# Kernel tuning notes

Measured on AMD Instinct MI355X. Metric: run time of the kernel, lower is better.

The kernel has to match this reference:

```python
import jax, jax.numpy as jnp
import numpy as np
from jax import lax

NMS_RADIUS = 4
THRESHOLD = 0.005
BORDER = 4
MAX_KP = 1024


def _max_pool(x, r):
    # torch max_pool2d pads with -inf; reduce_window 'SAME' pads with init value.
    w = 2 * r + 1
    return lax.reduce_window(x, -jnp.inf, lax.max, (1, w, w), (1, 1, 1), 'SAME')


def simple_nms(scores, radius):
    zeros = jnp.zeros_like(scores)
    max_mask = scores == _max_pool(scores, radius)
    for _ in range(2):
        supp_mask = _max_pool(max_mask.astype(scores.dtype), radius) > 0
        supp_scores = jnp.where(supp_mask, zeros, scores)
        new_max_mask = supp_scores == _max_pool(supp_scores, radius)
        max_mask = max_mask | (new_max_mask & ~supp_mask)
    return jnp.where(max_mask, scores, zeros)


def sample_descriptors(kp, desc, s):
    """Bilinear grid_sample (align_corners=True, zero padding) + L2 normalize.
    kp: [B,N,2] (x,y) full-resolution pixel coords; desc: [B,C,h,w]."""
    b, c, h, w = desc.shape
    k = kp - s / 2 + 0.5
    gx = k[..., 0] / (w * s - 1) * 2.0 - 1.0
    gy = k[..., 1] / (h * s - 1) * 2.0 - 1.0
    x = (gx + 1.0) * 0.5 * (w - 1)  # align_corners=True mapping
    y = (gy + 1.0) * 0.5 * (h - 1)
    x0 = jnp.floor(x); y0 = jnp.floor(y)
    wx1 = x - x0; wy1 = y - y0
    x0i = x0.astype(jnp.int32); y0i = y0.astype(jnp.int32)

    def tap(d_b, xi, yi):  # d_b [C,h,w]; xi,yi [N] -> [C,N], zero outside
        v = ((xi >= 0) & (xi < w) & (yi >= 0) & (yi < h)).astype(d_b.dtype)
        g = d_b[:, jnp.clip(yi, 0, h - 1), jnp.clip(xi, 0, w - 1)]
        return g * v

    def one(d_b, x0i, y0i, wx1, wy1):
        wx0 = 1.0 - wx1; wy0 = 1.0 - wy1
        return (tap(d_b, x0i, y0i) * (wx0 * wy0)
                + tap(d_b, x0i + 1, y0i) * (wx1 * wy0)
                + tap(d_b, x0i, y0i + 1) * (wx0 * wy1)
                + tap(d_b, x0i + 1, y0i + 1) * (wx1 * wy1))

    out = jax.vmap(one)(desc, x0i, y0i, wx1, wy1)  # [B,C,N]
    n = jnp.maximum(jnp.linalg.norm(out, axis=1, keepdims=True), 1e-12)
    return out / n


def conv1x1(w, b, x):  # Conv1d kernel_size=1: [O,I] @ [B,I,N]
    return jnp.einsum('oi,bin->bon', w, x) + b[None, :, None]


def setup_inputs() -> dict:
    key = jax.random.key(0)
    ks = jax.random.split(key, 13)
    B, H, W = 4, 480, 640
    inp = {
        'scores': jax.random.uniform(ks[0], (B, H, W), jnp.float32),
        'd1': jax.random.normal(ks[1], (B, 64, H // 2, W // 2), jnp.float32),
        'd2': jax.random.normal(ks[2], (B, 128, H // 4, W // 4), jnp.float32),
        'cDa': jax.random.normal(ks[3], (B, 256, H // 8, W // 8), jnp.float32),
        'd4': jax.random.normal(ks[4], (B, 256, H // 16, W // 16), jnp.float32),
        'lin0_w': jax.random.normal(ks[5], (256, 256), jnp.float32) / np.sqrt(256),
        'lin0_b': jax.random.normal(ks[6], (256,), jnp.float32) * 0.01,
        'lin1_w': jax.random.normal(ks[7], (128, 128), jnp.float32) / np.sqrt(128),
        'lin1_b': jax.random.normal(ks[8], (128,), jnp.float32) * 0.01,
        'lin2_w': jax.random.normal(ks[9], (64, 64), jnp.float32) / np.sqrt(64),
        'lin2_b': jax.random.normal(ks[10], (64,), jnp.float32) * 0.01,
        'merge_w': jax.random.normal(ks[11], (256, 704), jnp.float32) / np.sqrt(704),
        'merge_b': jax.random.normal(ks[12], (256,), jnp.float32) * 0.01,
    }
    return inp


def reference(scores, d1, d2, cDa, d4, lin0_w, lin0_b, lin1_w, lin1_b,
              lin2_w, lin2_b, merge_w, merge_b):
    B, H, W = scores.shape
    s = simple_nms(scores, NMS_RADIUS)
    ys, xs = jnp.meshgrid(jnp.arange(H), jnp.arange(W), indexing='ij')
    valid = (ys >= BORDER) & (ys < H - BORDER) & (xs >= BORDER) & (xs < W - BORDER)
    masked = jnp.where(valid[None] & (s > THRESHOLD), s, -1.0)
    top_scores, idx = lax.top_k(masked.reshape(B, -1), MAX_KP)
    kx = (idx % W).astype(jnp.float32)
    ky = (idx // W).astype(jnp.float32)
    kp = jnp.stack([kx, ky], axis=-1)  # [B,K,2] (x,y), i.e. torch.flip(k,[1])
    de1 = sample_descriptors(kp, d1, 2)    # [B,64,K]
    de2 = sample_descriptors(kp, d2, 4)    # [B,128,K]
    de3 = sample_descriptors(kp, cDa, 8)   # [B,256,K]
    de4 = sample_descriptors(kp, d4, 16)   # [B,256,K]
    de4 = conv1x1(lin0_w, lin0_b, de4)
    de2 = conv1x1(lin1_w, lin1_b, de2)
    de1 = conv1x1(lin2_w, lin2_b, de1)
    descriptors = conv1x1(merge_w, merge_b,
                          jnp.concatenate([de1, de2, de3, de4], axis=1))
    return kp, top_scores, descriptors
```

## Files before the change

kernel.cpp:

```cpp
#include <hip/hip_runtime.h>
#include <hip/hip_bf16.h>

#define B 4
#define H 480
#define W 640
#define HW (H*W)
#define BHW (B*H*W)
#define NKP 1024
#define THRESH 0.005f
#define CAP 16384
#define NCOL (B*NKP)
#define KTOT 704

typedef __attribute__((ext_vector_type(8))) short s8v;
typedef __attribute__((ext_vector_type(4))) float f4v;
typedef struct { float x, y; } __attribute__((aligned(4))) f2u;

__device__ __forceinline__ short f2bf(float f) {
    __hip_bfloat16 h = __float2bfloat16(f);
    return *(short*)&h;
}

__device__ __forceinline__ float max3f(float a, float b, float c) {
    return fmaxf(fmaxf(a, b), c);
}
#define MAX9(A, base, str) \
    max3f(max3f((A)[(base)], (A)[(base)+(str)], (A)[(base)+2*(str)]), \
          max3f((A)[(base)+3*(str)], (A)[(base)+4*(str)], (A)[(base)+5*(str)]), \
          max3f((A)[(base)+6*(str)], (A)[(base)+7*(str)], (A)[(base)+8*(str)]))

__global__ __launch_bounds__(256) void fuse_w(const float* __restrict__ merge_w,
                                              const float* __restrict__ lin0_w,
                                              const float* __restrict__ lin1_w,
                                              const float* __restrict__ lin2_w,
                                              short* __restrict__ Mw) {
    __shared__ float red[4][64];
    int lane = threadIdx.x & 63;
    int wv = threadIdx.x >> 6;
    int jb = blockIdx.x;
    int o = blockIdx.y;
    int j = jb * 64 + lane;
    const float* mwr = merge_w + (size_t)o * KTOT;

    if (jb >= 3 && jb <= 6) {
        if (wv == 0) Mw[(size_t)o * KTOT + j] = f2bf(mwr[j]);
        return;
    }
    float acc = 0.0f;
    if (jb == 0) {
        int k0 = wv * 16;
        #pragma unroll
        for (int k = 0; k < 16; ++k)
            acc += mwr[k0 + k] * lin2_w[(k0 + k) * 64 + lane];
    } else if (jb <= 2) {
        int jj = (jb - 1) * 64 + lane;
        int k0 = wv * 32;
        #pragma unroll
        for (int k = 0; k < 32; ++k)
            acc += mwr[64 + k0 + k] * lin1_w[(k0 + k) * 128 + jj];
    } else {
        int jj = (jb - 7) * 64 + lane;
        int k0 = wv * 64;
        #pragma unroll
        for (int k = 0; k < 64; ++k)
            acc += mwr[448 + k0 + k] * lin0_w[(k0 + k) * 256 + jj];
    }
    red[wv][lane] = acc;
    __syncthreads();
    if (wv == 0) {
        float t = red[0][lane] + red[1][lane] + red[2][lane] + red[3][lane];
        Mw[(size_t)o * KTOT + j] = f2bf(t);
    }
}

__global__ __launch_bounds__(256) void fuse_bias(const float* __restrict__ merge_w,
                                                 const float* __restrict__ merge_b,
                                                 const float* __restrict__ lin0_b,
                                                 const float* __restrict__ lin1_b,
                                                 const float* __restrict__ lin2_b,
                                                 float* __restrict__ biasf,
                                                 int* __restrict__ cnt) {
    int lane = threadIdx.x & 63;
    int wv = threadIdx.x >> 6;
    int o = blockIdx.x * 4 + wv;
    if (blockIdx.x == 0 && threadIdx.x < 4) cnt[threadIdx.x * 64] = 0;
    const float* mwr = merge_w + (size_t)o * KTOT;
    float acc = 0.0f;
    #pragma unroll
    for (int i = 0; i < 11; ++i) {
        int k = i * 64 + lane;
        float c;
        if (k < 64) c = lin2_b[k];
        else if (k < 192) c = lin1_b[k - 64];
        else if (k < 448) c = 0.0f;
        else c = lin0_b[k - 448];
        acc += mwr[k] * c;
    }
    #pragma unroll
    for (int off = 32; off > 0; off >>= 1) acc += __shfl_xor(acc, off, 64);
    if (lane == 0) biasf[o] = merge_b[o] + acc;
}

__global__ __launch_bounds__(256) void transpose_d4(const float* __restrict__ d4,
                                                    float* __restrict__ d4T) {
    __shared__ float T[64][65];
    int b = blockIdx.z;
    int p0 = blockIdx.x * 64;
    int c0 = blockIdx.y * 64;
    for (int t = threadIdx.x; t < 4096; t += 256) {
        int ch = t >> 6, px = t & 63;
        int gp = p0 + px;
        if (gp < 1200)
            T[ch][px] = d4[((size_t)(b * 256 + c0 + ch)) * 1200 + gp];
    }
    __syncthreads();
    for (int t = threadIdx.x; t < 4096; t += 256) {
        int px = t >> 6, ch = t & 63;
        int gp = p0 + px;
        if (gp < 1200)
            d4T[((size_t)(b * 1200 + gp)) * 256 + c0 + ch] = T[ch][px];
    }
}

__global__ __launch_bounds__(256) void transpose_cDa(const float* __restrict__ cDa,
                                                     float* __restrict__ cDaT) {
    __shared__ float T[64][65];
    int b = blockIdx.z;
    int p0 = blockIdx.x * 64;
    int c0 = blockIdx.y * 64;
    for (int t = threadIdx.x; t < 4096; t += 256) {
        int ch = t >> 6, px = t & 63;
        T[ch][px] = cDa[((size_t)(b * 256 + c0 + ch)) * 4800 + p0 + px];
    }
    __syncthreads();
    for (int t = threadIdx.x; t < 4096; t += 256) {
        int px = t >> 6, ch = t & 63;
        cDaT[((size_t)(b * 4800 + p0 + px)) * 256 + c0 + ch] = T[ch][px];
    }
}

__global__ __launch_bounds__(512) void nms_fused(const float* __restrict__ scores,
                                                 unsigned long long* __restrict__ cand,
                                                 int* __restrict__ cnt) {
    __shared__ float S72[72 * 72];
    __shared__ float T72[72 * 64];
    __shared__ float Mm[64 * 64];
    __shared__ float Zm[56 * 56];
    __shared__ int lcnt, gbase;
    int bz = blockIdx.z;
    int x0 = blockIdx.x * 32, y0 = blockIdx.y * 32;
    const float* sp = scores + bz * HW;
    if (threadIdx.x == 0) lcnt = 0;
    for (int t = threadIdx.x; t < 5184; t += 512) {
        int i = t / 72, j = t - i * 72;
        int gy = y0 - 20 + i, gx = x0 - 20 + j;
        S72[t] = (gy >= 0 && gy < H && gx >= 0 && gx < W) ? sp[gy * W + gx] : -1.0f;
    }
    __syncthreads();
    for (int t = threadIdx.x; t < 4608; t += 512) {
        int i = t >> 6, c = t & 63;
        T72[i * 64 + c] = MAX9(S72, i * 72 + c, 1);
    }
    __syncthreads();
    for (int t = threadIdx.x; t < 4096; t += 512) {
        int r = t >> 6, c = t & 63;
        float m = MAX9(T72, r * 64 + c, 64);
        float s = S72[(r + 4) * 72 + c + 4];
        int gy = y0 - 16 + r, gx = x0 - 16 + c;
        Mm[t] = (gy >= 0 && gy < H && gx >= 0 && gx < W && s == m) ? 1.0f : 0.0f;
    }
    __syncthreads();
    float* Tm = T72;
    for (int t = threadIdx.x; t < 3584; t += 512) {
        int i = t / 56, c = t - i * 56;
        Tm[i * 56 + c] = MAX9(Mm, i * 64 + c, 1);
    }
    __syncthreads();
    for (int t = threadIdx.x; t < 3136; t += 512) {
        int i = t / 56, j = t - i * 56;
        float m = MAX9(Tm, i * 56 + j, 56);
        Zm[t] = (m > 0.0f) ? -1.0f : S72[(i + 8) * 72 + (j + 8)];
    }
    __syncthreads();
    for (int t = threadIdx.x; t < 2688; t += 512) {
        int i = t / 48, c = t - i * 48;
        Tm[i * 56 + c] = MAX9(Zm, i * 56 + c, 1);
    }
    __syncthreads();
    for (int t = threadIdx.x; t < 2304; t += 512) {
        int r = t / 48, c = t - r * 48;
        float m = MAX9(Tm, r * 56 + c, 56);
        float Zc = Zm[(r + 4) * 56 + c + 4];
        int mi = (r + 8) * 64 + c + 8;
        bool nm = (Zc == m) && (Zc >= 0.0f);
        Mm[mi] = (Mm[mi] != 0.0f || nm) ? 1.0f : 0.0f;
    }
    __syncthreads();
    for (int t = threadIdx.x; t < 1920; t += 512) {
        int r = t / 40, c = t - r * 40;
        Tm[r * 56 + c] = MAX9(Mm, (r + 8) * 64 + c + 8, 1);
    }
    __syncthreads();
    for (int t = threadIdx.x; t < 1600; t += 512) {
        int r = t / 40, c = t - r * 40;
        float m = MAX9(Tm, r * 56 + c, 56);
        int zi = (r + 8) * 56 + c + 8;
        Zm[zi] = (m > 0.0f) ? -1.0f : S72[(r + 16) * 72 + (c + 16)];
    }
    __syncthreads();
    for (int t = threadIdx.x; t < 1280; t += 512) {
        int r = t / 32, c = t & 31;
        Tm[r * 56 + c] = MAX9(Zm, (r + 8) * 56 + c + 8, 1);
    }
    __syncthreads();
    unsigned long long keys[2];
    int nl = 0;
    #pragma unroll
    for (int q = 0; q < 2; ++q) {
        int t = threadIdx.x + q * 512;
        int r3 = t >> 5, c = t & 31;
        float m = MAX9(Tm, r3 * 56 + c, 56);
        float Zc = Zm[(r3 + 12) * 56 + c + 12];
        bool fin = (Mm[(r3 + 16) * 64 + c + 16] != 0.0f) || ((Zc == m) && (Zc >= 0.0f));
        int gy = y0 + r3, gx = x0 + c;
        float sc = S72[(r3 + 20) * 72 + (c + 20)];
        if (fin && gy >= 4 && gy < H - 4 && gx >= 4 && gx < W - 4 && sc > THRESH) {
            unsigned r = (unsigned)(gy * W + gx);
            unsigned bits = __float_as_uint(sc) | 0x80000000u;
            keys[nl++] = ((unsigned long long)bits << 32) |
                         (unsigned long long)(0xFFFFFFFFu - r);
        }
    }
    int lpos = 0;
    if (nl) lpos = atomicAdd(&lcnt, nl);
    __syncthreads();
    if (threadIdx.x == 0) gbase = (lcnt > 0) ? atomicAdd(&cnt[bz * 64], lcnt) : 0;
    __syncthreads();
    for (int j = 0; j < nl; ++j) {
        int p = gbase + lpos + j;
        if (p < CAP) cand[(size_t)bz * CAP + p] = keys[j];
    }
}

__global__ __launch_bounds__(1024) void topk(const unsigned long long* __restrict__ cand,
                                             const int* __restrict__ cnt,
                                             float* __restrict__ out, int* __restrict__ fidx,
                                             int* __restrict__ perm) {
    __shared__ int hist[2048];
    __shared__ int wtot[16], wcarry[16];
    __shared__ unsigned long long buf[4096];
    __shared__ int scnt, spiv1, spiv2, sabove;
    int b = blockIdx.x, tid = threadIdx.x;
    int lane = tid & 63, wv = tid >> 6;
    int m = cnt[b * 64]; if (m > CAP) m = CAP;
    const unsigned long long* cb = cand + (size_t)b * CAP;
    int target = (m < 1024) ? m : 1024;

    hist[tid] = 0; hist[tid + 1024] = 0;
    if (tid == 0) { scnt = 0; spiv1 = 2048; spiv2 = 0; sabove = 0; }
    __syncthreads();
    for (int i = tid; i < m; i += 1024)
        atomicAdd(&hist[(int)(cb[i] >> 53) & 0x7FF], 1);
    __syncthreads();
    {
        int base = wv * 128;
        int a = hist[base + lane];
        int c = hist[base + 64 + lane];
        int as = a, cs = c;
        #pragma unroll
        for (int off = 1; off < 64; off <<= 1) {
            int t1 = __shfl_down(as, off, 64);
            if (lane + off < 64) as += t1;
            int t2 = __shfl_down(cs, off, 64);
            if (lane + off < 64) cs += t2;
        }
        int ctot = __shfl(cs, 0, 64);
        as += ctot;
        if (lane == 0) wtot[wv] = as;
        __syncthreads();
        if (wv == 0 && lane < 16) {
            int v = wtot[lane];
            #pragma unroll
            for (int off = 1; off < 16; off <<= 1) {
                int t1 = __shfl_down(v, off, 64);
                if (lane + off < 16) v += t1;
            }
            wcarry[lane] = v - wtot[lane];
        }
        __syncthreads();
        int carry = wcarry[wv];
        hist[base + lane] = as + carry;
        hist[base + 64 + lane] = cs + carry;
    }
    __syncthreads();
    if (target > 0) {
        for (int t = tid; t < 2048; t += 1024) {
            int c = hist[t];
            int cn = (t < 2047) ? hist[t + 1] : 0;
            if (c >= target && cn < target) { spiv1 = t; sabove = cn; }
        }
    }
    __syncthreads();
    int piv1 = spiv1;
    int target2 = target - sabove;
    hist[tid] = 0; hist[tid + 1024] = 0;
    __syncthreads();
    for (int i = tid; i < m; i += 1024) {
        unsigned long long k = cb[i];
        if (((int)(k >> 53) & 0x7FF) == piv1)
            atomicAdd(&hist[(int)(k >> 42) & 0x7FF], 1);
    }
    __syncthreads();
    {
        int base = wv * 128;
        int a = hist[base + lane];
        int c = hist[base + 64 + lane];
        int as = a, cs = c;
        #pragma unroll
        for (int off = 1; off < 64; off <<= 1) {
            int t1 = __shfl_down(as, off, 64);
            if (lane + off < 64) as += t1;
            int t2 = __shfl_down(cs, off, 64);
            if (lane + off < 64) cs += t2;
        }
        int ctot = __shfl(cs, 0, 64);
        as += ctot;
        if (lane == 0) wtot[wv] = as;
        __syncthreads();
        if (wv == 0 && lane < 16) {
            int v = wtot[lane];
            #pragma unroll
            for (int off = 1; off < 16; off <<= 1) {
                int t1 = __shfl_down(v, off, 64);
                if (lane + off < 16) v += t1;
            }
            wcarry[lane] = v - wtot[lane];
        }
        __syncthreads();
        int carry = wcarry[wv];
        hist[base + lane] = as + carry;
        hist[base + 64 + lane] = cs + carry;
    }
    __syncthreads();
    if (target > 0) {
        for (int t = tid; t < 2048; t += 1024) {
            int c = hist[t];
            int cn = (t < 2047) ? hist[t + 1] : 0;
            if (c >= target2 && cn < target2) spiv2 = t;
        }
    }
    __syncthreads();
    int piv2 = spiv2;
    for (int i = tid; i < m; i += 1024) {
        unsigned long long k = cb[i];
        int b1 = (int)(k >> 53) & 0x7FF;
        bool sel = (target > 0) &&
                   (b1 > piv1 || (b1 == piv1 && (((int)(k >> 42) & 0x7FF) >= piv2)));
        if (sel) {
            int p = atomicAdd(&scnt, 1);
            if (p < 4096) buf[p] = k;
        }
    }
    __syncthreads();
    int sc_ = scnt; if (sc_ > 4096) sc_ = 4096;
    int ns = 1024; while (ns < sc_) ns <<= 1;
    for (int t = tid; t < ns; t += 1024) if (t >= sc_) buf[t] = 0ULL;
    __syncthreads();
    int nseg = ns >> 6;
    for (int seg = wv; seg < nseg; seg += 16) {
        int e = (seg << 6) + lane;
        unsigned long long v = buf[e];
        #pragma unroll
        for (int k = 2; k <= 64; k <<= 1) {
            #pragma unroll
            for (int j = k >> 1; j >= 1; j >>= 1) {
                unsigned long long p = __shfl_xor(v, j, 64);
                bool upper = (lane & j) != 0;
                bool dird = ((e & k) == 0);
                bool keepmax = (dird != upper);
                v = keepmax ? (v > p ? v : p) : (v < p ? v : p);
            }
        }
        buf[e] = v;
    }
    for (int k = 128; k <= ns; k <<= 1) {
        for (int j = k >> 1; j >= 64; j >>= 1) {
            __syncthreads();
            for (int t = tid; t < ns; t += 1024) {
                int ixj = t ^ j;
                if (ixj > t) {
                    unsigned long long a = buf[t], bb = buf[ixj];
                    if (((t & k) == 0) ? (a < bb) : (a > bb)) { buf[t] = bb; buf[ixj] = a; }
                }
            }
        }
        __syncthreads();
        for (int seg = wv; seg < nseg; seg += 16) {
            int e = (seg << 6) + lane;
            unsigned long long v = buf[e];
            #pragma unroll
            for (int j = 32; j >= 1; j >>= 1) {
                unsigned long long p = __shfl_xor(v, j, 64);
                bool upper = (lane & j) != 0;
                bool dird = ((e & k) == 0);
                bool keepmax = (dird != upper);
                v = keepmax ? (v > p ? v : p) : (v < p ? v : p);
            }
            buf[e] = v;
        }
    }
    __syncthreads();
    unsigned long long key = buf[tid];
    float kx, ky, sc;
    unsigned idx;
    if (key != 0ULL) {
        unsigned ord = (unsigned)(key >> 32);
        sc = __uint_as_float(ord ^ 0x80000000u);
        idx = 0xFFFFFFFFu - (unsigned)(key & 0xFFFFFFFFu);
        kx = (float)(idx % W);
        ky = (float)(idx / W);
    } else {
        sc = -1.0f; idx = 0; kx = 0.0f; ky = 0.0f;
    }
    int bn = b * NKP + tid;
    out[bn * 2 + 0] = kx;
    out[bn * 2 + 1] = ky;
    out[B * NKP * 2 + bn] = sc;
    fidx[bn] = (int)idx;
    __syncthreads();
    if (tid < 512) { hist[tid] = 0; hist[tid + 1024] = 0; }
    __syncthreads();
    int bucket = (int)(idx >> 10);
    atomicAdd(&hist[bucket], 1);
    __syncthreads();
    int iv = 0;
    if (wv < 8) {
        iv = hist[wv * 64 + lane];
        #pragma unroll
        for (int off = 1; off < 64; off <<= 1) {
            int t1 = __shfl_up(iv, off, 64);
            if (lane >= off) iv += t1;
        }
        if (lane == 63) wtot[wv] = iv;
    }
    __syncthreads();
    if (wv == 0 && lane < 8) {
        int v = wtot[lane], iv2 = v;
        #pragma unroll
        for (int off = 1; off < 8; off <<= 1) {
            int t1 = __shfl_up(iv2, off, 64);
            if (lane >= off) iv2 += t1;
        }
        wcarry[lane] = iv2 - v;
    }
    __syncthreads();
    if (wv < 8) hist[512 + wv * 64 + lane] = iv + wcarry[wv];
    __syncthreads();
    int intra = atomicAdd(&hist[1024 + bucket], 1);
    int pos = hist[512 + bucket] - hist[bucket] + intra;
    perm[b * NKP + pos] = tid;
}

__global__ __launch_bounds__(256) void sample_all(const float* __restrict__ d1,
                                                  const float* __restrict__ d2,
                                                  const float* __restrict__ cDa,
                                                  const float* __restrict__ d4T,
                                                  const float* __restrict__ cDaT,
                                                  const int* __restrict__ fidx,
                                                  const int* __restrict__ perm,
                                                  short* __restrict__ X) {
    int lane = threadIdx.x & 63;
    int wv = threadIdx.x >> 6;
    int seg = blockIdx.y;
    int bid = blockIdx.x;
    int swz = ((bid & 7) << 7) | (bid >> 3);
    int b = swz >> 8;
    int g0 = ((swz & 255) << 2) + wv;

    const float* map; int h, w, s, C, base, nset;
    if (seg == 0)      { map = d1;  h = 240; w = 320; s = 2;  C = 64;  base = 0;   nset = 1; }
    else if (seg == 1) { map = d2;  h = 120; w = 160; s = 4;  C = 128; base = 64;  nset = 2; }
    else if (seg == 2) { map = cDa; h = 60;  w = 80;  s = 8;  C = 256; base = 192; nset = 4; }
    else               { map = d4T; h = 30;  w = 40;  s = 16; C = 256; base = 448; nset = 4; }

    int col = (b << 10) | perm[(b << 10) + g0];
    int idx = fidx[col];
    float kx = (float)(idx % W);
    float ky = (float)(idx / W);
    float kxs = kx - (float)s * 0.5f + 0.5f;
    float kys = ky - (float)s * 0.5f + 0.5f;
    float gx = kxs / (float)(w * s - 1) * 2.0f - 1.0f;
    float gy = kys / (float)(h * s - 1) * 2.0f - 1.0f;
    float x = (gx + 1.0f) * 0.5f * (float)(w - 1);
    float y = (gy + 1.0f) * 0.5f * (float)(h - 1);
    float x0f = floorf(x), y0f = floorf(y);
    int x0 = (int)x0f, y0 = (int)y0f;
    float wx1 = x - x0f, wy1 = y - y0f;
    float wx0 = 1.0f - wx1, wy0 = 1.0f - wy1;
    bool vx0 = (x0 >= 0) && (x0 < w);
    bool vx1 = (x0 + 1 >= 0) && (x0 + 1 < w);
    bool vy0 = (y0 >= 0) && (y0 < h);
    bool vy1 = (y0 + 1 >= 0) && (y0 + 1 < h);
    int xc0 = min(max(x0, 0), w - 1), xc1 = min(max(x0 + 1, 0), w - 1);
    int yc0 = min(max(y0, 0), h - 1), yc1 = min(max(y0 + 1, 0), h - 1);
    float w00 = (vx0 && vy0) ? wx0 * wy0 : 0.0f;
    float w01 = (vx1 && vy0) ? wx1 * wy0 : 0.0f;
    float w10 = (vx0 && vy1) ? wx0 * wy1 : 0.0f;
    float w11 = (vx1 && vy1) ? wx1 * wy1 : 0.0f;

    bool nhwc = (seg == 3) || (seg == 2 && cDaT != nullptr);
    float vals[4];
    float r = 0.0f;
    if (nhwc) {
        const float* pt;
        int wq;
        if (seg == 3) { pt = d4T + ((size_t)b * 1200) * 256 + lane; wq = 40; }
        else          { pt = cDaT + ((size_t)b * 4800) * 256 + lane; wq = 80; }
        size_t o00 = ((size_t)(yc0 * wq + xc0)) << 8;
        size_t o01 = ((size_t)(yc0 * wq + xc1)) << 8;
        size_t o10 = ((size_t)(yc1 * wq + xc0)) << 8;
        size_t o11 = ((size_t)(yc1 * wq + xc1)) << 8;
        float q00[4], q01[4], q10[4], q11[4];
        #pragma unroll
        for (int j = 0; j < 4; ++j) {
            q00[j] = pt[o00 + j * 64]; q01[j] = pt[o01 + j * 64];
            q10[j] = pt[o10 + j * 64]; q11[j] = pt[o11 + j * 64];
        }
        #pragma unroll
        for (int j = 0; j < 4; ++j) {
            vals[j] = q00[j] * w00 + q01[j] * w01 + q10[j] * w10 + q11[j] * w11;
            r += vals[j] * vals[j];
        }
    } else {
        int xb = min(xc0, w - 2);
        float s0 = (xc0 == xb) ? 1.0f : 0.0f;
        float s1 = (xc1 == xb) ? 1.0f : 0.0f;
        float ax = w00 * s0 + w01 * s1;
        float ay = w00 * (1.0f - s0) + w01 * (1.0f - s1);
        float bx = w10 * s0 + w11 * s1;
        float by = w10 * (1.0f - s0) + w11 * (1.0f - s1);
        size_t hw = (size_t)(h * w);
        const float* pb = map + ((size_t)b * C + lane) * hw;
        size_t off0 = (size_t)yc0 * w + xb;
        size_t off1 = (size_t)yc1 * w + xb;
        size_t cstr = hw << 6;
        f2u q0[4], q1[4];
        #pragma unroll
        for (int j = 0; j < 4; ++j) {
            if (j < nset) {
                const float* p = pb + (size_t)j * cstr;
                q0[j] = *(const f2u*)(p + off0);
                q1[j] = *(const f2u*)(p + off1);
            }
        }
        #pragma unroll
        for (int j = 0; j < 4; ++j) {
            if (j < nset) {
                vals[j] = q0[j].x * ax + q0[j].y * ay + q1[j].x * bx + q1[j].y * by;
                r += vals[j] * vals[j];
            }
        }
    }
    #pragma unroll
    for (int off = 32; off > 0; off >>= 1) r += __shfl_xor(r, off, 64);
    float denom = fmaxf(sqrtf(r), 1e-12f);
    float inv = 1.0f / denom;
    short* xp = X + (size_t)col * KTOT + base + lane;
    #pragma unroll
    for (int j = 0; j < 4; ++j) {
        if (j < nset) xp[j * 64] = f2bf(vals[j] * inv);
    }
}

__global__ __launch_bounds__(256) void gemm_mfma(const short* __restrict__ Mw,
                                                 const short* __restrict__ X,
                                                 const float* __restrict__ biasf,
                                                 float* __restrict__ out) {
    __shared__ short As[64 * 72];
    __shared__ short Bs[64 * 72];
    int tid = threadIdx.x;
    int lane = tid & 63, w = tid >> 6;
    int r = lane & 15, quad = lane >> 4;
    int rowBase = blockIdx.y * 64, colBase = blockIdx.x * 64;
    int sm = tid >> 2, skq = (tid & 3) << 4;

    const short* pa = Mw + (size_t)(rowBase + sm) * KTOT + skq;
    const short* pb = X + (size_t)(colBase + sm) * KTOT + skq;
    s8v a0 = *(const s8v*)(pa), a1 = *(const s8v*)(pa + 8);
    s8v b0 = *(const s8v*)(pb), b1 = *(const s8v*)(pb + 8);

    f4v acc[4];
    #pragma unroll
    for (int t = 0; t < 4; ++t) acc[t] = (f4v)0.0f;

    for (int kt = 0; kt < 11; ++kt) {
        __syncthreads();
        *(s8v*)&As[sm * 72 + skq + 0] = a0;
        *(s8v*)&As[sm * 72 + skq + 8] = a1;
        *(s8v*)&Bs[sm * 72 + skq + 0] = b0;
        *(s8v*)&Bs[sm * 72 + skq + 8] = b1;
        __syncthreads();
        if (kt < 10) {
            pa += 64; pb += 64;
            a0 = *(const s8v*)(pa); a1 = *(const s8v*)(pa + 8);
            b0 = *(const s8v*)(pb); b1 = *(const s8v*)(pb + 8);
        }
        #pragma unroll
        for (int kk = 0; kk < 2; ++kk) {
            int aoff = (w * 16 + r) * 72 + kk * 32 + quad * 8;
            s8v af = *(const s8v*)&As[aoff];
            #pragma unroll
            for (int t = 0; t < 4; ++t) {
                int boff = (t * 16 + r) * 72 + kk * 32 + quad * 8;
                s8v bf = *(const s8v*)&Bs[boff];
                acc[t] = __builtin_amdgcn_mfma_f32_16x16x32_bf16(af, bf, acc[t], 0, 0, 0);
            }
        }
    }
    #pragma unroll
    for (int t = 0; t < 4; ++t) {
        int colg = colBase + t * 16 + r;
        size_t obase = (size_t)(colg >> 10) * (256 * NKP) + (size_t)(colg & 1023);
        #pragma unroll
        for (int reg = 0; reg < 4; ++reg) {
            int row = rowBase + w * 16 + quad * 4 + reg;
            out[obase + (size_t)row * NKP] = acc[t][reg] + biasf[row];
        }
    }
}

extern "C" void kernel_launch(void* const* d_in, const int* in_sizes, int n_in,
                              void* d_out, int out_size, void* d_ws, size_t ws_size,
                              hipStream_t stream) {
    const float* scores  = (const float*)d_in[0];
    const float* d1      = (const float*)d_in[1];
    const float* d2      = (const float*)d_in[2];
    const float* cDa     = (const float*)d_in[3];
    const float* d4      = (const float*)d_in[4];
    const float* lin0_w  = (const float*)d_in[5];
    const float* lin0_b  = (const float*)d_in[6];
    const float* lin1_w  = (const float*)d_in[7];
    const float* lin1_b  = (const float*)d_in[8];
    const float* lin2_w  = (const float*)d_in[9];
    const float* lin2_b  = (const float*)d_in[10];
    const float* merge_w = (const float*)d_in[11];
    const float* merge_b = (const float*)d_in[12];
    float* out = (float*)d_out;

    char* ws = (char*)d_ws;
    short* Xbuf = (short*)ws;
    float* d4T  = (float*)(ws + 6291456);
    unsigned long long* cand  = (unsigned long long*)(ws + 14745600);
    int* cnt                  = (int*)(ws + 15269888);
    int* fidx                 = (int*)(ws + 15401984);
    short* Mw                 = (short*)(ws + 15418368);
    float* biasf              = (float*)(ws + 16139264);
    int* perm                 = (int*)(ws + 16140288);
    float* cDaT = nullptr;
    if (ws_size >= 16156672ULL + 19660800ULL)
        cDaT = (float*)(ws + 16156672);

    dim3 tgrid(W / 32, H / 32, B);

    fuse_w<<<dim3(11, 256), 256, 0, stream>>>(merge_w, lin0_w, lin1_w, lin2_w, Mw);
    fuse_bias<<<64, 256, 0, stream>>>(merge_w, merge_b, lin0_b, lin1_b, lin2_b, biasf, cnt);
    transpose_d4<<<dim3(19, 4, 4), 256, 0, stream>>>(d4, d4T);
    if (cDaT)
        transpose_cDa<<<dim3(75, 4, 4), 256, 0, stream>>>(cDa, cDaT);
    nms_fused<<<tgrid, 512, 0, stream>>>(scores, cand, cnt);
    topk<<<B, 1024, 0, stream>>>(cand, cnt, out, fidx, perm);
    sample_all<<<dim3(1024, 4), 256, 0, stream>>>(d1, d2, cDa, d4T, cDaT, fidx, perm, Xbuf);
    gemm_mfma<<<dim3(NCOL / 64, 256 / 64), 256, 0, stream>>>(Mw, Xbuf, biasf, out + B * NKP * 3);
}
```

Before: 296.6 us.

## Transpose d2 to channel-last for coalesced sampling and widen NMS blocks

Adds a transpose kernel that converts the d2 feature map (128 channels, 120x160) into NHWC layout in extra workspace. The sampler then reads d2 through the channel-contiguous gather path already used for the other maps, instead of the strided NCHW path. NMS blocks also grow from 512 to 1024 threads, so each thread produces at most one candidate. The cost is a full extra read and write of d2 every call, and the new path only runs if the workspace is large enough.

```diff
diff --git a/kernel.cpp b/kernel.cpp
--- a/kernel.cpp
+++ b/kernel.cpp
@@ -139,9 +139,26 @@
     }
 }
 
-__global__ __launch_bounds__(512) void nms_fused(const float* __restrict__ scores,
-                                                 unsigned long long* __restrict__ cand,
-                                                 int* __restrict__ cnt) {
+__global__ __launch_bounds__(256) void transpose_d2(const float* __restrict__ d2,
+                                                    float* __restrict__ d2T) {
+    __shared__ float T[64][65];
+    int b = blockIdx.z;
+    int p0 = blockIdx.x * 64;
+    int c0 = blockIdx.y * 64;
+    for (int t = threadIdx.x; t < 4096; t += 256) {
+        int ch = t >> 6, px = t & 63;
+        T[ch][px] = d2[((size_t)(b * 128 + c0 + ch)) * 19200 + p0 + px];
+    }
+    __syncthreads();
+    for (int t = threadIdx.x; t < 4096; t += 256) {
+        int px = t >> 6, ch = t & 63;
+        d2T[((size_t)(b * 19200 + p0 + px)) * 128 + c0 + ch] = T[ch][px];
+    }
+}
+
+__global__ __launch_bounds__(1024, 8) void nms_fused(const float* __restrict__ scores,
+                                                     unsigned long long* __restrict__ cand,
+                                                     int* __restrict__ cnt) {
     __shared__ float S72[72 * 72];
     __shared__ float T72[72 * 64];
     __shared__ float Mm[64 * 64];
@@ -151,18 +168,18 @@
     int x0 = blockIdx.x * 32, y0 = blockIdx.y * 32;
     const float* sp = scores + bz * HW;
     if (threadIdx.x == 0) lcnt = 0;
-    for (int t = threadIdx.x; t < 5184; t += 512) {
+    for (int t = threadIdx.x; t < 5184; t += 1024) {
         int i = t / 72, j = t - i * 72;
         int gy = y0 - 20 + i, gx = x0 - 20 + j;
         S72[t] = (gy >= 0 && gy < H && gx >= 0 && gx < W) ? sp[gy * W + gx] : -1.0f;
     }
     __syncthreads();
-    for (int t = threadIdx.x; t < 4608; t += 512) {
+    for (int t = threadIdx.x; t < 4608; t += 1024) {
         int i = t >> 6, c = t & 63;
         T72[i * 64 + c] = MAX9(S72, i * 72 + c, 1);
     }
     __syncthreads();
-    for (int t = threadIdx.x; t < 4096; t += 512) {
+    for (int t = threadIdx.x; t < 4096; t += 1024) {
         int r = t >> 6, c = t & 63;
         float m = MAX9(T72, r * 64 + c, 64);
         float s = S72[(r + 4) * 72 + c + 4];
@@ -171,23 +188,23 @@
     }
     __syncthreads();
     float* Tm = T72;
-    for (int t = threadIdx.x; t < 3584; t += 512) {
+    for (int t = threadIdx.x; t < 3584; t += 1024) {
         int i = t / 56, c = t - i * 56;
         Tm[i * 56 + c] = MAX9(Mm, i * 64 + c, 1);
     }
     __syncthreads();
-    for (int t = threadIdx.x; t < 3136; t += 512) {
+    for (int t = threadIdx.x; t < 3136; t += 1024) {
         int i = t / 56, j = t - i * 56;
         float m = MAX9(Tm, i * 56 + j, 56);
         Zm[t] = (m > 0.0f) ? -1.0f : S72[(i + 8) * 72 + (j + 8)];
     }
     __syncthreads();
-    for (int t = threadIdx.x; t < 2688; t += 512) {
+    for (int t = threadIdx.x; t < 2688; t += 1024) {
         int i = t / 48, c = t - i * 48;
         Tm[i * 56 + c] = MAX9(Zm, i * 56 + c, 1);
     }
     __syncthreads();
-    for (int t = threadIdx.x; t < 2304; t += 512) {
+    for (int t = threadIdx.x; t < 2304; t += 1024) {
         int r = t / 48, c = t - r * 48;
         float m = MAX9(Tm, r * 56 + c, 56);
         float Zc = Zm[(r + 4) * 56 + c + 4];
@@ -196,28 +213,27 @@
         Mm[mi] = (Mm[mi] != 0.0f || nm) ? 1.0f : 0.0f;
     }
     __syncthreads();
-    for (int t = threadIdx.x; t < 1920; t += 512) {
+    for (int t = threadIdx.x; t < 1920; t += 1024) {
         int r = t / 40, c = t - r * 40;
         Tm[r * 56 + c] = MAX9(Mm, (r + 8) * 64 + c + 8, 1);
     }
     __syncthreads();
-    for (int t = threadIdx.x; t < 1600; t += 512) {
+    for (int t = threadIdx.x; t < 1600; t += 1024) {
         int r = t / 40, c = t - r * 40;
         float m = MAX9(Tm, r * 56 + c, 56);
         int zi = (r + 8) * 56 + c + 8;
         Zm[zi] = (m > 0.0f) ? -1.0f : S72[(r + 16) * 72 + (c + 16)];
     }
     __syncthreads();
-    for (int t = threadIdx.x; t < 1280; t += 512) {
+    for (int t = threadIdx.x; t < 1280; t += 1024) {
         int r = t / 32, c = t & 31;
         Tm[r * 56 + c] = MAX9(Zm, (r + 8) * 56 + c + 8, 1);
     }
     __syncthreads();
-    unsigned long long keys[2];
+    unsigned long long key0 = 0ULL;
     int nl = 0;
-    #pragma unroll
-    for (int q = 0; q < 2; ++q) {
-        int t = threadIdx.x + q * 512;
+    {
+        int t = threadIdx.x;
         int r3 = t >> 5, c = t & 31;
         float m = MAX9(Tm, r3 * 56 + c, 56);
         float Zc = Zm[(r3 + 12) * 56 + c + 12];
@@ -227,18 +243,19 @@
         if (fin && gy >= 4 && gy < H - 4 && gx >= 4 && gx < W - 4 && sc > THRESH) {
             unsigned r = (unsigned)(gy * W + gx);
             unsigned bits = __float_as_uint(sc) | 0x80000000u;
-            keys[nl++] = ((unsigned long long)bits << 32) |
-                         (unsigned long long)(0xFFFFFFFFu - r);
+            key0 = ((unsigned long long)bits << 32) |
+                   (unsigned long long)(0xFFFFFFFFu - r);
+            nl = 1;
         }
     }
     int lpos = 0;
-    if (nl) lpos = atomicAdd(&lcnt, nl);
+    if (nl) lpos = atomicAdd(&lcnt, 1);
     __syncthreads();
     if (threadIdx.x == 0) gbase = (lcnt > 0) ? atomicAdd(&cnt[bz * 64], lcnt) : 0;
     __syncthreads();
-    for (int j = 0; j < nl; ++j) {
-        int p = gbase + lpos + j;
-        if (p < CAP) cand[(size_t)bz * CAP + p] = keys[j];
+    if (nl) {
+        int p = gbase + lpos;
+        if (p < CAP) cand[(size_t)bz * CAP + p] = key0;
     }
 }
 
@@ -466,6 +483,7 @@
                                                   const float* __restrict__ cDa,
                                                   const float* __restrict__ d4T,
                                                   const float* __restrict__ cDaT,
+                                                  const float* __restrict__ d2T,
                                                   const int* __restrict__ fidx,
                                                   const int* __restrict__ perm,
                                                   short* __restrict__ X) {
@@ -508,28 +526,32 @@
     float w10 = (vx0 && vy1) ? wx0 * wy1 : 0.0f;
     float w11 = (vx1 && vy1) ? wx1 * wy1 : 0.0f;
 
-    bool nhwc = (seg == 3) || (seg == 2 && cDaT != nullptr);
+    bool nhwc = (seg == 3) || (seg == 2 && cDaT != nullptr) || (seg == 1 && d2T != nullptr);
     float vals[4];
     float r = 0.0f;
     if (nhwc) {
-        const float* pt;
-        int wq;
-        if (seg == 3) { pt = d4T + ((size_t)b * 1200) * 256 + lane; wq = 40; }
-        else          { pt = cDaT + ((size_t)b * 4800) * 256 + lane; wq = 80; }
-        size_t o00 = ((size_t)(yc0 * wq + xc0)) << 8;
-        size_t o01 = ((size_t)(yc0 * wq + xc1)) << 8;
-        size_t o10 = ((size_t)(yc1 * wq + xc0)) << 8;
-        size_t o11 = ((size_t)(yc1 * wq + xc1)) << 8;
+        const float* pt; int wq, Cc;
+        if (seg == 3)      { pt = d4T + ((size_t)b * 1200) * 256 + lane;  wq = 40;  Cc = 256; }
+        else if (seg == 2) { pt = cDaT + ((size_t)b * 4800) * 256 + lane; wq = 80;  Cc = 256; }
+        else               { pt = d2T + ((size_t)b * 19200) * 128 + lane; wq = 160; Cc = 128; }
+        size_t o00 = (size_t)(yc0 * wq + xc0) * Cc;
+        size_t o01 = (size_t)(yc0 * wq + xc1) * Cc;
+        size_t o10 = (size_t)(yc1 * wq + xc0) * Cc;
+        size_t o11 = (size_t)(yc1 * wq + xc1) * Cc;
         float q00[4], q01[4], q10[4], q11[4];
         #pragma unroll
         for (int j = 0; j < 4; ++j) {
-            q00[j] = pt[o00 + j * 64]; q01[j] = pt[o01 + j * 64];
-            q10[j] = pt[o10 + j * 64]; q11[j] = pt[o11 + j * 64];
+            if (j < nset) {
+                q00[j] = pt[o00 + j * 64]; q01[j] = pt[o01 + j * 64];
+                q10[j] = pt[o10 + j * 64]; q11[j] = pt[o11 + j * 64];
+            }
         }
         #pragma unroll
         for (int j = 0; j < 4; ++j) {
-            vals[j] = q00[j] * w00 + q01[j] * w01 + q10[j] * w10 + q11[j] * w11;
-            r += vals[j] * vals[j];
+            if (j < nset) {
+                vals[j] = q00[j] * w00 + q01[j] * w01 + q10[j] * w10 + q11[j] * w11;
+                r += vals[j] * vals[j];
+            }
         }
     } else {
         int xb = min(xc0, w - 2);
@@ -657,8 +679,11 @@
     float* biasf              = (float*)(ws + 16139264);
     int* perm                 = (int*)(ws + 16140288);
     float* cDaT = nullptr;
+    float* d2T  = nullptr;
     if (ws_size >= 16156672ULL + 19660800ULL)
         cDaT = (float*)(ws + 16156672);
+    if (ws_size >= 35817472ULL + 39321600ULL)
+        d2T = (float*)(ws + 35817472);
 
     dim3 tgrid(W / 32, H / 32, B);
 
@@ -667,8 +692,11 @@
     transpose_d4<<<dim3(19, 4, 4), 256, 0, stream>>>(d4, d4T);
     if (cDaT)
         transpose_cDa<<<dim3(75, 4, 4), 256, 0, stream>>>(cDa, cDaT);
-    nms_fused<<<tgrid, 512, 0, stream>>>(scores, cand, cnt);
+    if (d2T)
+        transpose_d2<<<dim3(300, 2, 4), 256, 0, stream>>>(d2, d2T);
+    nms_fused<<<tgrid, 1024, 0, stream>>>(scores, cand, cnt);
     topk<<<B, 1024, 0, stream>>>(cand, cnt, out, fidx, perm);
-    sample_all<<<dim3(1024, 4), 256, 0, stream>>>(d1, d2, cDa, d4T, cDaT, fidx, perm, Xbuf);
+    sample_all<<<dim3(1024, 4), 256, 0, stream>>>(d1, d2, cDa, d4T, cDaT, d2T,
+                                                  fidx, perm, Xbuf);
     gemm_mfma<<<dim3(NCOL / 64, 256 / 64), 256, 0, stream>>>(Mw, Xbuf, biasf, out + B * NKP * 3);
 }
```

After: 297.7 us. About the same (+0.4%).
